# Optimization experiments

Measured on AMD Instinct MI355X. Metric: run time of the kernel, lower is better.

Reference implementation:

```python
import jax, jax.numpy as jnp
import numpy as np
from jax import lax

B_SZ, L, D, N = 4, 2048, 768, 16


def setup_inputs() -> dict:
    key = jax.random.key(0)
    ks = jax.random.split(key, 8)
    x = jax.random.normal(ks[0], (B_SZ, L, D), dtype=jnp.float32)
    # A_log init: log(repeat(arange(1, N+1), 'n -> d n'))
    A_log = jnp.log(jnp.tile(jnp.arange(1, N + 1, dtype=jnp.float32), (D, 1)))  # (D, N)
    sD = 1.0 / np.sqrt(D)
    Wb = jax.random.normal(ks[1], (N, D), dtype=jnp.float32) * sD
    bb = jax.random.normal(ks[2], (N,), dtype=jnp.float32) * sD
    Wc = jax.random.normal(ks[3], (N, D), dtype=jnp.float32) * sD
    bc = jax.random.normal(ks[4], (N,), dtype=jnp.float32) * sD
    W1 = jax.random.normal(ks[5], (1, D), dtype=jnp.float32) * sD
    b1 = jnp.zeros((1,), dtype=jnp.float32)
    Wd = jax.random.normal(ks[6], (D, 1), dtype=jnp.float32)
    bd = jax.random.normal(ks[7], (D,), dtype=jnp.float32)
    return {"x": x, "A_log": A_log, "Wb": Wb, "bb": bb, "Wc": Wc, "bc": bc,
            "W1": W1, "b1": b1, "Wd": Wd, "bd": bd}


def reference(x, A_log, Wb, bb, Wc, bc, W1, b1, Wd, bd):
    # x: (b, l, d)
    A = -jnp.exp(A_log)                                   # (d, n)
    Bp = x @ Wb.T + bb                                    # (b, l, n)
    C = x @ Wc.T + bc                                     # (b, l, n)
    s1 = x @ W1.T + b1                                    # (b, l, 1)
    delta = jax.nn.softplus(s1 @ Wd.T + bd)               # (b, l, d)
    deltaA = jnp.exp(jnp.einsum('bld,dn->bldn', delta, A))          # (b, l, d, n)
    deltaB_u = jnp.einsum('bld,bln,bld->bldn', delta, Bp, x)        # (b, l, d, n)

    def step(h, inputs):
        dA, dBu, c = inputs                               # (b,d,n),(b,d,n),(b,n)
        h = dA * h + dBu
        y = jnp.einsum('bdn,bn->bd', h, c)
        return h, y

    b, l, d = x.shape
    n = A_log.shape[1]
    h0 = jnp.zeros((b, d, n), dtype=x.dtype)
    _, ys = lax.scan(step, h0, (jnp.moveaxis(deltaA, 1, 0),
                                jnp.moveaxis(deltaB_u, 1, 0),
                                jnp.moveaxis(C, 1, 0)))
    return jnp.moveaxis(ys, 0, 1)                          # (b, l, d)
```

## Files before the change

### kernel.cpp

```cpp
#include <hip/hip_runtime.h>
#include <math.h>

#define B_SZ 4
#define LSEQ 2048
#define DDIM 768
#define NST  16
#define NROW (B_SZ * LSEQ)
#define NJ   33

#define NC   128
#define CS   (LSEQ / NC)

#define KSPL 32
#define KCH  (DDIM / KSPL)

__global__ __launch_bounds__(256) void proj_part_kernel(
    const float* __restrict__ x,
    const float* __restrict__ Wb, const float* __restrict__ Wc,
    const float* __restrict__ W1, float* __restrict__ part)
{
    const int row = blockIdx.x * 256 + threadIdx.x;
    const int s = blockIdx.y;
    const int k0 = s * KCH;

    float4 xv[6];
    const float* xp = x + (size_t)row * DDIM + k0;
    #pragma unroll
    for (int q = 0; q < 6; ++q) xv[q] = *(const float4*)(xp + q * 4);

    float acc[NJ];
    #pragma unroll
    for (int j = 0; j < NJ; ++j) {
        const float* wrow = (j < 16) ? (Wb + j * DDIM)
                          : (j < 32) ? (Wc + (j - 16) * DDIM)
                                     : W1;
        const float* wk = wrow + k0;
        float a = 0.f;
        #pragma unroll
        for (int q = 0; q < 6; ++q) {
            a = fmaf(xv[q].x, wk[q * 4 + 0], a);
            a = fmaf(xv[q].y, wk[q * 4 + 1], a);
            a = fmaf(xv[q].z, wk[q * 4 + 2], a);
            a = fmaf(xv[q].w, wk[q * 4 + 3], a);
        }
        acc[j] = a;
    }
    #pragma unroll
    for (int j = 0; j < NJ; ++j)
        part[((size_t)s * NJ + j) * NROW + row] = acc[j];
}

__global__ __launch_bounds__(256) void proj_reduce_kernel(
    const float* __restrict__ part,
    const float* __restrict__ bb, const float* __restrict__ bc,
    const float* __restrict__ b1,
    float* __restrict__ Bp, float* __restrict__ Cc, float* __restrict__ s1)
{
    const int idx = blockIdx.x * 256 + threadIdx.x;
    if (idx >= NJ * NROW) return;
    const int j = idx / NROW;
    const int row = idx % NROW;
    float a = 0.f;
    #pragma unroll 8
    for (int s = 0; s < KSPL; ++s)
        a += part[((size_t)s * NJ + j) * NROW + row];
    if (j < 16)      Bp[(size_t)row * NST + j] = a + bb[j];
    else if (j < 32) Cc[(size_t)row * NST + (j - 16)] = a + bc[j - 16];
    else             s1[row] = a + b1[0];
}

__device__ __forceinline__ float softplus_f(float z) {
    float t = __expf(-fabsf(z));
    return fmaxf(z, 0.f) + __logf(1.f + t);
}

__device__ __forceinline__ void powers16(float p, float* e) {
    e[0] = p;      e[1] = p * p;      e[2] = e[1] * p;   e[3] = e[1] * e[1];
    e[4] = e[3] * p;  e[5] = e[3] * e[1];  e[6] = e[3] * e[2];  e[7] = e[3] * e[3];
    e[8] = e[7] * p;  e[9] = e[7] * e[1];  e[10] = e[7] * e[2]; e[11] = e[7] * e[3];
    e[12] = e[7] * e[4]; e[13] = e[7] * e[5]; e[14] = e[7] * e[6]; e[15] = e[7] * e[7];
}

__device__ __forceinline__ bool a_structured(const float* acoef) {
    bool st = true;
    #pragma unroll
    for (int n = 0; n < NST; ++n)
        st = st && (fabsf(acoef[n] - (float)(n + 1) * acoef[0]) <= 1e-5f * fabsf(acoef[n]));
    return __all(st) != 0;
}

__global__ __launch_bounds__(256) void pass1_kernel(
    const float* __restrict__ x, const float* __restrict__ A_log,
    const float* __restrict__ Wd, const float* __restrict__ bd,
    const float* __restrict__ Bp, const float* __restrict__ s1,
    float* __restrict__ Ssum, float* __restrict__ Q)
{
    const int tid = threadIdx.x;
    const int d = blockIdx.x * 256 + tid;
    const int c = blockIdx.y, b = blockIdx.z;
    const int rowbase = b * LSEQ + c * CS;

    const float wd = Wd[d], bdv = bd[d];
    float acoef[NST];
    #pragma unroll
    for (int n = 0; n < NST; ++n) acoef[n] = -__expf(A_log[d * NST + n]);
    const float a0 = acoef[0];
    const bool structured = a_structured(acoef);

    const float4* B4 = (const float4*)(Bp + (size_t)rowbase * NST);
    const float* s1p = s1 + rowbase;
    const float* xp = x + (size_t)rowbase * DDIM + d;

    float h[NST];
    #pragma unroll
    for (int n = 0; n < NST; ++n) h[n] = 0.f;
    float S = 0.f;

    if (structured) {
        #pragma unroll 4
        for (int l = 0; l < CS; ++l) {
            const float delta = softplus_f(fmaf(s1p[l], wd, bdv));
            S += delta;
            float e[NST];
            powers16(__expf(delta * a0), e);
            const float dx = delta * xp[(size_t)l * DDIM];
            const float4 b0 = B4[l * 4 + 0], b1v = B4[l * 4 + 1];
            const float4 b2 = B4[l * 4 + 2], b3v = B4[l * 4 + 3];
            const float bv[NST] = {b0.x, b0.y, b0.z, b0.w, b1v.x, b1v.y, b1v.z, b1v.w,
                                   b2.x, b2.y, b2.z, b2.w, b3v.x, b3v.y, b3v.z, b3v.w};
            #pragma unroll
            for (int n = 0; n < NST; ++n) h[n] = fmaf(e[n], h[n], dx * bv[n]);
        }
    } else {
        #pragma unroll 4
        for (int l = 0; l < CS; ++l) {
            const float delta = softplus_f(fmaf(s1p[l], wd, bdv));
            S += delta;
            float e[NST];
            #pragma unroll
            for (int n = 0; n < NST; ++n) e[n] = __expf(delta * acoef[n]);
            const float dx = delta * xp[(size_t)l * DDIM];
            const float4 b0 = B4[l * 4 + 0], b1v = B4[l * 4 + 1];
            const float4 b2 = B4[l * 4 + 2], b3v = B4[l * 4 + 3];
            const float bv[NST] = {b0.x, b0.y, b0.z, b0.w, b1v.x, b1v.y, b1v.z, b1v.w,
                                   b2.x, b2.y, b2.z, b2.w, b3v.x, b3v.y, b3v.z, b3v.w};
            #pragma unroll
            for (int n = 0; n < NST; ++n) h[n] = fmaf(e[n], h[n], dx * bv[n]);
        }
    }
    Ssum[((size_t)b * NC + c) * DDIM + d] = S;
    const size_t gbase = (((size_t)b * NC + c) * DDIM + d) * NST;
    float4* Q4 = (float4*)(Q + gbase);
    #pragma unroll
    for (int q = 0; q < 4; ++q)
        Q4[q] = make_float4(h[q * 4], h[q * 4 + 1], h[q * 4 + 2], h[q * 4 + 3]);
}

#define CPG (NC / 4)
__global__ __launch_bounds__(256) void combine_kernel(
    const float* __restrict__ A_log,
    const float* __restrict__ Ssum, const float* __restrict__ Q,
    float* __restrict__ Hin)
{
    const int gidx = blockIdx.x * 256 + threadIdx.x;
    const int lane = threadIdx.x & 63;
    const int rlow = gidx & 15;
    const int g = (gidx >> 4) & 3;
    const int hi = gidx >> 6;
    const int pairIdx = hi * 16 + rlow;
    const int b = pairIdx / (DDIM * NST);
    const int r = pairIdx % (DDIM * NST);
    const int d = r >> 4;
    const float acoef = -__expf(A_log[r]);
    const int c0 = g * CPG;

    float eq[CPG], qq[CPG];
    #pragma unroll
    for (int ci = 0; ci < CPG; ++ci) {
        const size_t base = (size_t)(b * NC + c0 + ci);
        eq[ci] = __expf(acoef * Ssum[base * DDIM + d]);
        qq[ci] = Q[base * (DDIM * NST) + r];
    }
    float E = 1.f, H = 0.f;
    #pragma unroll
    for (int ci = 0; ci < CPG; ++ci) { H = fmaf(eq[ci], H, qq[ci]); E *= eq[ci]; }

    float oE = __shfl_up(E, 16, 64);
    float oH = __shfl_up(H, 16, 64);
    if (lane >= 16) { H = fmaf(E, oH, H); E *= oE; }
    oE = __shfl_up(E, 32, 64);
    oH = __shfl_up(H, 32, 64);
    if (lane >= 32) { H = fmaf(E, oH, H); E *= oE; }

    float hin = __shfl_up(H, 16, 64);
    if (g == 0) hin = 0.f;

    float h = hin;
    #pragma unroll
    for (int ci = 0; ci < CPG; ++ci) {
        const size_t base = (size_t)(b * NC + c0 + ci);
        Hin[base * (DDIM * NST) + r] = h;
        h = fmaf(eq[ci], h, qq[ci]);
    }
}

__global__ __launch_bounds__(256) void pass2_kernel(
    const float* __restrict__ x, const float* __restrict__ A_log,
    const float* __restrict__ Wd, const float* __restrict__ bd,
    const float* __restrict__ Bp, const float* __restrict__ Cc,
    const float* __restrict__ s1, const float* __restrict__ Hin,
    float* __restrict__ out)
{
    const int tid = threadIdx.x;
    const int d = blockIdx.x * 256 + tid;
    const int c = blockIdx.y, b = blockIdx.z;
    const int rowbase = b * LSEQ + c * CS;

    const float wd = Wd[d], bdv = bd[d];
    float acoef[NST];
    #pragma unroll
    for (int n = 0; n < NST; ++n) acoef[n] = -__expf(A_log[d * NST + n]);
    const float a0 = acoef[0];
    const bool structured = a_structured(acoef);

    const float4* B4 = (const float4*)(Bp + (size_t)rowbase * NST);
    const float4* C4 = (const float4*)(Cc + (size_t)rowbase * NST);
    const float* s1p = s1 + rowbase;
    const float* xp = x + (size_t)rowbase * DDIM + d;
    float* yp = out + (size_t)rowbase * DDIM + d;

    float h[NST];
    const size_t gbase = (((size_t)b * NC + c) * DDIM + d) * NST;
    const float4* H4 = (const float4*)(Hin + gbase);
    #pragma unroll
    for (int q = 0; q < 4; ++q) {
        const float4 hv = H4[q];
        h[q * 4] = hv.x; h[q * 4 + 1] = hv.y; h[q * 4 + 2] = hv.z; h[q * 4 + 3] = hv.w;
    }

    if (structured) {
        #pragma unroll 4
        for (int l = 0; l < CS; ++l) {
            const float delta = softplus_f(fmaf(s1p[l], wd, bdv));
            float e[NST];
            powers16(__expf(delta * a0), e);
            const float dx = delta * xp[(size_t)l * DDIM];
            const float4 b0 = B4[l * 4 + 0], b1v = B4[l * 4 + 1];
            const float4 b2 = B4[l * 4 + 2], b3v = B4[l * 4 + 3];
            const float4 c0 = C4[l * 4 + 0], c1v = C4[l * 4 + 1];
            const float4 c2 = C4[l * 4 + 2], c3v = C4[l * 4 + 3];
            const float bv[NST] = {b0.x, b0.y, b0.z, b0.w, b1v.x, b1v.y, b1v.z, b1v.w,
                                   b2.x, b2.y, b2.z, b2.w, b3v.x, b3v.y, b3v.z, b3v.w};
            const float cv[NST] = {c0.x, c0.y, c0.z, c0.w, c1v.x, c1v.y, c1v.z, c1v.w,
                                   c2.x, c2.y, c2.z, c2.w, c3v.x, c3v.y, c3v.z, c3v.w};
            float y = 0.f;
            #pragma unroll
            for (int n = 0; n < NST; ++n) {
                h[n] = fmaf(e[n], h[n], dx * bv[n]);
                y = fmaf(h[n], cv[n], y);
            }
            yp[(size_t)l * DDIM] = y;
        }
    } else {
        #pragma unroll 4
        for (int l = 0; l < CS; ++l) {
            const float delta = softplus_f(fmaf(s1p[l], wd, bdv));
            float e[NST];
            #pragma unroll
            for (int n = 0; n < NST; ++n) e[n] = __expf(delta * acoef[n]);
            const float dx = delta * xp[(size_t)l * DDIM];
            const float4 b0 = B4[l * 4 + 0], b1v = B4[l * 4 + 1];
            const float4 b2 = B4[l * 4 + 2], b3v = B4[l * 4 + 3];
            const float4 c0 = C4[l * 4 + 0], c1v = C4[l * 4 + 1];
            const float4 c2 = C4[l * 4 + 2], c3v = C4[l * 4 + 3];
            const float bv[NST] = {b0.x, b0.y, b0.z, b0.w, b1v.x, b1v.y, b1v.z, b1v.w,
                                   b2.x, b2.y, b2.z, b2.w, b3v.x, b3v.y, b3v.z, b3v.w};
            const float cv[NST] = {c0.x, c0.y, c0.z, c0.w, c1v.x, c1v.y, c1v.z, c1v.w,
                                   c2.x, c2.y, c2.z, c2.w, c3v.x, c3v.y, c3v.z, c3v.w};
            float y = 0.f;
            #pragma unroll
            for (int n = 0; n < NST; ++n) {
                h[n] = fmaf(e[n], h[n], dx * bv[n]);
                y = fmaf(h[n], cv[n], y);
            }
            yp[(size_t)l * DDIM] = y;
        }
    }
}

extern "C" void kernel_launch(void* const* d_in, const int* in_sizes, int n_in,
                              void* d_out, int out_size, void* d_ws, size_t ws_size,
                              hipStream_t stream) {
    const float* x     = (const float*)d_in[0];
    const float* A_log = (const float*)d_in[1];
    const float* Wb    = (const float*)d_in[2];
    const float* bb    = (const float*)d_in[3];
    const float* Wc    = (const float*)d_in[4];
    const float* bc    = (const float*)d_in[5];
    const float* W1    = (const float*)d_in[6];
    const float* b1    = (const float*)d_in[7];
    const float* Wd    = (const float*)d_in[8];
    const float* bd    = (const float*)d_in[9];
    float* out = (float*)d_out;

    float* ws = (float*)d_ws;
    const size_t partN = (size_t)KSPL * NJ * NROW;
    const size_t BpN = (size_t)NROW * NST;
    const size_t s1N = (size_t)NROW;
    const size_t sN  = (size_t)B_SZ * NC * DDIM;
    const size_t agg = (size_t)B_SZ * NC * DDIM * NST;

    float* part = ws;
    float* Bp   = part + partN;
    float* Cc   = Bp + BpN;
    float* s1   = Cc + BpN;
    float* Ssum = s1 + s1N;
    float* Q    = Ssum + sN;
    float* Hin  = Q + agg;

    dim3 gproj(NROW / 256, KSPL);
    proj_part_kernel<<<gproj, 256, 0, stream>>>(x, Wb, Wc, W1, part);
    proj_reduce_kernel<<<(NJ * NROW + 255) / 256, 256, 0, stream>>>(part, bb, bc, b1, Bp, Cc, s1);

    dim3 gscan(DDIM / 256, NC, B_SZ);
    pass1_kernel<<<gscan, 256, 0, stream>>>(x, A_log, Wd, bd, Bp, s1, Ssum, Q);

    combine_kernel<<<(B_SZ * DDIM * NST * 4) / 256, 256, 0, stream>>>(A_log, Ssum, Q, Hin);

    pass2_kernel<<<gscan, 256, 0, stream>>>(x, A_log, Wd, bd, Bp, Cc, s1, Hin, out);
}
```

Measured before the change: 155.1 us.

## Fuse chunked scan passes into one cooperative kernel with grid syncs

Merges pass1, combine and pass2 into a single cooperative kernel that uses grid-wide syncs between phases. This removes two kernel launch boundaries and computes A coefficients once per thread. To make the grid fit co-resident, the chunk count is halved to 64, which gives longer sequential chunks and fewer parallel blocks. The projection K-split is also halved. A fallback runs the old three-kernel path when cooperative launch is unavailable.

```diff
diff --git a/kernel.cpp b/kernel.cpp
--- a/kernel.cpp
+++ b/kernel.cpp
@@ -1,5 +1,8 @@
 #include <hip/hip_runtime.h>
+#include <hip/hip_cooperative_groups.h>
 #include <math.h>
+
+namespace cg = cooperative_groups;
 
 #define B_SZ 4
 #define LSEQ 2048
@@ -8,10 +11,11 @@
 #define NROW (B_SZ * LSEQ)
 #define NJ   33
 
-#define NC   128
+#define NC   64
 #define CS   (LSEQ / NC)
-
-#define KSPL 32
+#define CPG  (NC / 4)
+
+#define KSPL 16
 #define KCH  (DDIM / KSPL)
 
 __global__ __launch_bounds__(256) void proj_part_kernel(
@@ -23,10 +27,10 @@
     const int s = blockIdx.y;
     const int k0 = s * KCH;
 
-    float4 xv[6];
+    float4 xv[KCH / 4];
     const float* xp = x + (size_t)row * DDIM + k0;
     #pragma unroll
-    for (int q = 0; q < 6; ++q) xv[q] = *(const float4*)(xp + q * 4);
+    for (int q = 0; q < KCH / 4; ++q) xv[q] = *(const float4*)(xp + q * 4);
 
     float acc[NJ];
     #pragma unroll
@@ -37,7 +41,7 @@
         const float* wk = wrow + k0;
         float a = 0.f;
         #pragma unroll
-        for (int q = 0; q < 6; ++q) {
+        for (int q = 0; q < KCH / 4; ++q) {
             a = fmaf(xv[q].x, wk[q * 4 + 0], a);
             a = fmaf(xv[q].y, wk[q * 4 + 1], a);
             a = fmaf(xv[q].z, wk[q * 4 + 2], a);
@@ -61,7 +65,7 @@
     const int j = idx / NROW;
     const int row = idx % NROW;
     float a = 0.f;
-    #pragma unroll 8
+    #pragma unroll
     for (int s = 0; s < KSPL; ++s)
         a += part[((size_t)s * NJ + j) * NROW + row];
     if (j < 16)      Bp[(size_t)row * NST + j] = a + bb[j];
@@ -89,24 +93,15 @@
     return __all(st) != 0;
 }
 
-__global__ __launch_bounds__(256) void pass1_kernel(
-    const float* __restrict__ x, const float* __restrict__ A_log,
-    const float* __restrict__ Wd, const float* __restrict__ bd,
+__device__ __forceinline__ void phaseA_body(
+    int b, int c, int d,
+    const float* __restrict__ x, const float* __restrict__ Wd, const float* __restrict__ bd,
     const float* __restrict__ Bp, const float* __restrict__ s1,
+    const float* acoef, float a0, bool structured,
     float* __restrict__ Ssum, float* __restrict__ Q)
 {
-    const int tid = threadIdx.x;
-    const int d = blockIdx.x * 256 + tid;
-    const int c = blockIdx.y, b = blockIdx.z;
     const int rowbase = b * LSEQ + c * CS;
-
     const float wd = Wd[d], bdv = bd[d];
-    float acoef[NST];
-    #pragma unroll
-    for (int n = 0; n < NST; ++n) acoef[n] = -__expf(A_log[d * NST + n]);
-    const float a0 = acoef[0];
-    const bool structured = a_structured(acoef);
-
     const float4* B4 = (const float4*)(Bp + (size_t)rowbase * NST);
     const float* s1p = s1 + rowbase;
     const float* xp = x + (size_t)rowbase * DDIM + d;
@@ -156,29 +151,27 @@
         Q4[q] = make_float4(h[q * 4], h[q * 4 + 1], h[q * 4 + 2], h[q * 4 + 3]);
 }
 
-#define CPG (NC / 4)
-__global__ __launch_bounds__(256) void combine_kernel(
+__device__ __forceinline__ void phaseB_body(
+    int gidx, int lane,
     const float* __restrict__ A_log,
     const float* __restrict__ Ssum, const float* __restrict__ Q,
     float* __restrict__ Hin)
 {
-    const int gidx = blockIdx.x * 256 + threadIdx.x;
-    const int lane = threadIdx.x & 63;
     const int rlow = gidx & 15;
     const int g = (gidx >> 4) & 3;
     const int hi = gidx >> 6;
     const int pairIdx = hi * 16 + rlow;
-    const int b = pairIdx / (DDIM * NST);
+    const int b2 = pairIdx / (DDIM * NST);
     const int r = pairIdx % (DDIM * NST);
-    const int d = r >> 4;
-    const float acoef = -__expf(A_log[r]);
+    const int d2 = r >> 4;
+    const float ac = -__expf(A_log[r]);
     const int c0 = g * CPG;
 
     float eq[CPG], qq[CPG];
     #pragma unroll
     for (int ci = 0; ci < CPG; ++ci) {
-        const size_t base = (size_t)(b * NC + c0 + ci);
-        eq[ci] = __expf(acoef * Ssum[base * DDIM + d]);
+        const size_t base = (size_t)(b2 * NC + c0 + ci);
+        eq[ci] = __expf(ac * Ssum[base * DDIM + d2]);
         qq[ci] = Q[base * (DDIM * NST) + r];
     }
     float E = 1.f, H = 0.f;
@@ -198,31 +191,22 @@
     float h = hin;
     #pragma unroll
     for (int ci = 0; ci < CPG; ++ci) {
-        const size_t base = (size_t)(b * NC + c0 + ci);
+        const size_t base = (size_t)(b2 * NC + c0 + ci);
         Hin[base * (DDIM * NST) + r] = h;
         h = fmaf(eq[ci], h, qq[ci]);
     }
 }
 
-__global__ __launch_bounds__(256) void pass2_kernel(
-    const float* __restrict__ x, const float* __restrict__ A_log,
-    const float* __restrict__ Wd, const float* __restrict__ bd,
+__device__ __forceinline__ void phaseC_body(
+    int b, int c, int d,
+    const float* __restrict__ x, const float* __restrict__ Wd, const float* __restrict__ bd,
     const float* __restrict__ Bp, const float* __restrict__ Cc,
     const float* __restrict__ s1, const float* __restrict__ Hin,
+    const float* acoef, float a0, bool structured,
     float* __restrict__ out)
 {
-    const int tid = threadIdx.x;
-    const int d = blockIdx.x * 256 + tid;
-    const int c = blockIdx.y, b = blockIdx.z;
     const int rowbase = b * LSEQ + c * CS;
-
     const float wd = Wd[d], bdv = bd[d];
-    float acoef[NST];
-    #pragma unroll
-    for (int n = 0; n < NST; ++n) acoef[n] = -__expf(A_log[d * NST + n]);
-    const float a0 = acoef[0];
-    const bool structured = a_structured(acoef);
-
     const float4* B4 = (const float4*)(Bp + (size_t)rowbase * NST);
     const float4* C4 = (const float4*)(Cc + (size_t)rowbase * NST);
     const float* s1p = s1 + rowbase;
@@ -247,12 +231,12 @@
             const float dx = delta * xp[(size_t)l * DDIM];
             const float4 b0 = B4[l * 4 + 0], b1v = B4[l * 4 + 1];
             const float4 b2 = B4[l * 4 + 2], b3v = B4[l * 4 + 3];
-            const float4 c0 = C4[l * 4 + 0], c1v = C4[l * 4 + 1];
-            const float4 c2 = C4[l * 4 + 2], c3v = C4[l * 4 + 3];
+            const float4 c0v = C4[l * 4 + 0], c1v = C4[l * 4 + 1];
+            const float4 c2v = C4[l * 4 + 2], c3v = C4[l * 4 + 3];
             const float bv[NST] = {b0.x, b0.y, b0.z, b0.w, b1v.x, b1v.y, b1v.z, b1v.w,
                                    b2.x, b2.y, b2.z, b2.w, b3v.x, b3v.y, b3v.z, b3v.w};
-            const float cv[NST] = {c0.x, c0.y, c0.z, c0.w, c1v.x, c1v.y, c1v.z, c1v.w,
-                                   c2.x, c2.y, c2.z, c2.w, c3v.x, c3v.y, c3v.z, c3v.w};
+            const float cv[NST] = {c0v.x, c0v.y, c0v.z, c0v.w, c1v.x, c1v.y, c1v.z, c1v.w,
+                                   c2v.x, c2v.y, c2v.z, c2v.w, c3v.x, c3v.y, c3v.z, c3v.w};
             float y = 0.f;
             #pragma unroll
             for (int n = 0; n < NST; ++n) {
@@ -271,12 +255,12 @@
             const float dx = delta * xp[(size_t)l * DDIM];
             const float4 b0 = B4[l * 4 + 0], b1v = B4[l * 4 + 1];
             const float4 b2 = B4[l * 4 + 2], b3v = B4[l * 4 + 3];
-            const float4 c0 = C4[l * 4 + 0], c1v = C4[l * 4 + 1];
-            const float4 c2 = C4[l * 4 + 2], c3v = C4[l * 4 + 3];
+            const float4 c0v = C4[l * 4 + 0], c1v = C4[l * 4 + 1];
+            const float4 c2v = C4[l * 4 + 2], c3v = C4[l * 4 + 3];
             const float bv[NST] = {b0.x, b0.y, b0.z, b0.w, b1v.x, b1v.y, b1v.z, b1v.w,
                                    b2.x, b2.y, b2.z, b2.w, b3v.x, b3v.y, b3v.z, b3v.w};
-            const float cv[NST] = {c0.x, c0.y, c0.z, c0.w, c1v.x, c1v.y, c1v.z, c1v.w,
-                                   c2.x, c2.y, c2.z, c2.w, c3v.x, c3v.y, c3v.z, c3v.w};
+            const float cv[NST] = {c0v.x, c0v.y, c0v.z, c0v.w, c1v.x, c1v.y, c1v.z, c1v.w,
+                                   c2v.x, c2v.y, c2v.z, c2v.w, c3v.x, c3v.y, c3v.z, c3v.w};
             float y = 0.f;
             #pragma unroll
             for (int n = 0; n < NST; ++n) {
@@ -286,6 +270,85 @@
             yp[(size_t)l * DDIM] = y;
         }
     }
+}
+
+__global__ __launch_bounds__(256) void pass1_kernel(
+    const float* __restrict__ x, const float* __restrict__ A_log,
+    const float* __restrict__ Wd, const float* __restrict__ bd,
+    const float* __restrict__ Bp, const float* __restrict__ s1,
+    float* __restrict__ Ssum, float* __restrict__ Q)
+{
+    const int d = blockIdx.x * 256 + threadIdx.x;
+    const int c = blockIdx.y, b = blockIdx.z;
+    float acoef[NST];
+    #pragma unroll
+    for (int n = 0; n < NST; ++n) acoef[n] = -__expf(A_log[d * NST + n]);
+    const bool structured = a_structured(acoef);
+    phaseA_body(b, c, d, x, Wd, bd, Bp, s1, acoef, acoef[0], structured, Ssum, Q);
+}
+
+__global__ __launch_bounds__(256) void combine_kernel(
+    const float* __restrict__ A_log,
+    const float* __restrict__ Ssum, const float* __restrict__ Q,
+    float* __restrict__ Hin)
+{
+    const int gidx = blockIdx.x * 256 + threadIdx.x;
+    phaseB_body(gidx, threadIdx.x & 63, A_log, Ssum, Q, Hin);
+}
+
+__global__ __launch_bounds__(256) void pass2_kernel(
+    const float* __restrict__ x, const float* __restrict__ A_log,
+    const float* __restrict__ Wd, const float* __restrict__ bd,
+    const float* __restrict__ Bp, const float* __restrict__ Cc,
+    const float* __restrict__ s1, const float* __restrict__ Hin,
+    float* __restrict__ out)
+{
+    const int d = blockIdx.x * 256 + threadIdx.x;
+    const int c = blockIdx.y, b = blockIdx.z;
+    float acoef[NST];
+    #pragma unroll
+    for (int n = 0; n < NST; ++n) acoef[n] = -__expf(A_log[d * NST + n]);
+    const bool structured = a_structured(acoef);
+    phaseC_body(b, c, d, x, Wd, bd, Bp, Cc, s1, Hin, acoef, acoef[0], structured, out);
+}
+
+#define GRID_F (3 * B_SZ * NC)
+
+__global__ __launch_bounds__(256, 3) void fused_scan_kernel(
+    const float* __restrict__ x, const float* __restrict__ A_log,
+    const float* __restrict__ Wd, const float* __restrict__ bd,
+    const float* __restrict__ Bp, const float* __restrict__ Cc,
+    const float* __restrict__ s1,
+    float* __restrict__ Ssum, float* __restrict__ Q, float* __restrict__ Hin,
+    float* __restrict__ out)
+{
+    const int tid = threadIdx.x;
+    const int bx = blockIdx.x;
+    const int dblk = bx / (B_SZ * NC);
+    const int rem  = bx % (B_SZ * NC);
+    const int b    = rem / NC;
+    const int c    = rem % NC;
+    const int d    = dblk * 256 + tid;
+
+    float acoef[NST];
+    #pragma unroll
+    for (int n = 0; n < NST; ++n) acoef[n] = -__expf(A_log[d * NST + n]);
+    const float a0 = acoef[0];
+    const bool structured = a_structured(acoef);
+
+    phaseA_body(b, c, d, x, Wd, bd, Bp, s1, acoef, a0, structured, Ssum, Q);
+
+    __threadfence();
+    cg::this_grid().sync();
+    __threadfence();
+
+    phaseB_body(bx * 256 + tid, tid & 63, A_log, Ssum, Q, Hin);
+
+    __threadfence();
+    cg::this_grid().sync();
+    __threadfence();
+
+    phaseC_body(b, c, d, x, Wd, bd, Bp, Cc, s1, Hin, acoef, a0, structured, out);
 }
 
 extern "C" void kernel_launch(void* const* d_in, const int* in_sizes, int n_in,
@@ -322,10 +385,33 @@
     proj_part_kernel<<<gproj, 256, 0, stream>>>(x, Wb, Wc, W1, part);
     proj_reduce_kernel<<<(NJ * NROW + 255) / 256, 256, 0, stream>>>(part, bb, bc, b1, Bp, Cc, s1);
 
-    dim3 gscan(DDIM / 256, NC, B_SZ);
-    pass1_kernel<<<gscan, 256, 0, stream>>>(x, A_log, Wd, bd, Bp, s1, Ssum, Q);
-
-    combine_kernel<<<(B_SZ * DDIM * NST * 4) / 256, 256, 0, stream>>>(A_log, Ssum, Q, Hin);
-
-    pass2_kernel<<<gscan, 256, 0, stream>>>(x, A_log, Wd, bd, Bp, Cc, s1, Hin, out);
-}
+    static int coop_mode = -1;
+    if (coop_mode < 0) {
+        int dev = 0;
+        (void)hipGetDevice(&dev);
+        int coopAttr = 0;
+        (void)hipDeviceGetAttribute(&coopAttr, hipDeviceAttributeCooperativeLaunch, dev);
+        int ncu = 0;
+        (void)hipDeviceGetAttribute(&ncu, hipDeviceAttributeMultiprocessorCount, dev);
+        int nblk = 0;
+        hipError_t oe = hipOccupancyMaxActiveBlocksPerMultiprocessor(&nblk, fused_scan_kernel, 256, 0);
+        coop_mode = (coopAttr && oe == hipSuccess && (long)nblk * ncu >= GRID_F) ? 1 : 0;
+    }
+
+    bool done = false;
+    if (coop_mode == 1) {
+        void* kargs[] = {(void*)&x, (void*)&A_log, (void*)&Wd, (void*)&bd,
+                         (void*)&Bp, (void*)&Cc, (void*)&s1,
+                         (void*)&Ssum, (void*)&Q, (void*)&Hin, (void*)&out};
+        hipError_t le = hipLaunchCooperativeKernel((const void*)fused_scan_kernel,
+                                                   dim3(GRID_F), dim3(256), kargs, 0, stream);
+        if (le == hipSuccess) done = true;
+        else coop_mode = 0;
+    }
+    if (!done) {
+        dim3 gscan(DDIM / 256, NC, B_SZ);
+        pass1_kernel<<<gscan, 256, 0, stream>>>(x, A_log, Wd, bd, Bp, s1, Ssum, Q);
+        combine_kernel<<<(B_SZ * DDIM * NST * 4) / 256, 256, 0, stream>>>(A_log, Ssum, Q, Hin);
+        pass2_kernel<<<gscan, 256, 0, stream>>>(x, A_log, Wd, bd, Bp, Cc, s1, Hin, out);
+    }
+}
```

New measurement: 157.0 us. No clear change (+1.2%).

## Stage chunk inputs in shared memory and halve scan chunk and K-split counts

Applied to the files above, without the earlier changes.

The two scan passes now cooperatively load the chunk's x tile, B/C coefficients and s1 values into shared memory with vectorized float4 loads before the recurrence, instead of each thread issuing strided global loads per timestep. The chunk count drops from 128 to 64, giving longer chunks, a smaller Q/Hin aggregate buffer and a cheaper combine step. The projection K-split drops from 32 to 16, so each thread does more work per split and the partial-sum buffer and reduction shrink. In exchange there is less parallelism in the scan kernels, which may hurt latency hiding, and added LDS use (about 32KB per block) that limits occupancy.

```diff
diff --git a/kernel.cpp b/kernel.cpp
--- a/kernel.cpp
+++ b/kernel.cpp
@@ -8,10 +8,11 @@
 #define NROW (B_SZ * LSEQ)
 #define NJ   33
 
-#define NC   128
+#define NC   64
 #define CS   (LSEQ / NC)
-
-#define KSPL 32
+#define CPG  (NC / 4)
+
+#define KSPL 16
 #define KCH  (DDIM / KSPL)
 
 __global__ __launch_bounds__(256) void proj_part_kernel(
@@ -23,10 +24,10 @@
     const int s = blockIdx.y;
     const int k0 = s * KCH;
 
-    float4 xv[6];
+    float4 xv[KCH / 4];
     const float* xp = x + (size_t)row * DDIM + k0;
     #pragma unroll
-    for (int q = 0; q < 6; ++q) xv[q] = *(const float4*)(xp + q * 4);
+    for (int q = 0; q < KCH / 4; ++q) xv[q] = *(const float4*)(xp + q * 4);
 
     float acc[NJ];
     #pragma unroll
@@ -37,7 +38,7 @@
         const float* wk = wrow + k0;
         float a = 0.f;
         #pragma unroll
-        for (int q = 0; q < 6; ++q) {
+        for (int q = 0; q < KCH / 4; ++q) {
             a = fmaf(xv[q].x, wk[q * 4 + 0], a);
             a = fmaf(xv[q].y, wk[q * 4 + 1], a);
             a = fmaf(xv[q].z, wk[q * 4 + 2], a);
@@ -61,7 +62,7 @@
     const int j = idx / NROW;
     const int row = idx % NROW;
     float a = 0.f;
-    #pragma unroll 8
+    #pragma unroll
     for (int s = 0; s < KSPL; ++s)
         a += part[((size_t)s * NJ + j) * NROW + row];
     if (j < 16)      Bp[(size_t)row * NST + j] = a + bb[j];
@@ -95,10 +96,34 @@
     const float* __restrict__ Bp, const float* __restrict__ s1,
     float* __restrict__ Ssum, float* __restrict__ Q)
 {
+    __shared__ float xs[CS][256];
+    __shared__ float bs[CS][NST];
+    __shared__ float ss[CS];
+
     const int tid = threadIdx.x;
-    const int d = blockIdx.x * 256 + tid;
+    const int d0 = blockIdx.x * 256;
+    const int d = d0 + tid;
     const int c = blockIdx.y, b = blockIdx.z;
     const int rowbase = b * LSEQ + c * CS;
+
+    {
+        const float4* xg = (const float4*)(x + (size_t)rowbase * DDIM + d0);
+        #pragma unroll
+        for (int i = 0; i < (CS * 256 / 4) / 256; ++i) {
+            const int flat = i * 256 + tid;
+            const int r = flat >> 6, q = flat & 63;
+            const float4 v = xg[(size_t)r * (DDIM / 4) + q];
+            float* p = &xs[r][q * 4];
+            p[0] = v.x; p[1] = v.y; p[2] = v.z; p[3] = v.w;
+        }
+        if (tid < CS * NST / 4) {
+            const float4 v = ((const float4*)(Bp + (size_t)rowbase * NST))[tid];
+            const int r = tid >> 2, q = tid & 3;
+            float* p = &bs[r][q * 4];
+            p[0] = v.x; p[1] = v.y; p[2] = v.z; p[3] = v.w;
+        }
+        if (tid < CS) ss[tid] = s1[rowbase + tid];
+    }
 
     const float wd = Wd[d], bdv = bd[d];
     float acoef[NST];
@@ -107,9 +132,7 @@
     const float a0 = acoef[0];
     const bool structured = a_structured(acoef);
 
-    const float4* B4 = (const float4*)(Bp + (size_t)rowbase * NST);
-    const float* s1p = s1 + rowbase;
-    const float* xp = x + (size_t)rowbase * DDIM + d;
+    __syncthreads();
 
     float h[NST];
     #pragma unroll
@@ -119,13 +142,15 @@
     if (structured) {
         #pragma unroll 4
         for (int l = 0; l < CS; ++l) {
-            const float delta = softplus_f(fmaf(s1p[l], wd, bdv));
+            const float delta = softplus_f(fmaf(ss[l], wd, bdv));
             S += delta;
             float e[NST];
             powers16(__expf(delta * a0), e);
-            const float dx = delta * xp[(size_t)l * DDIM];
-            const float4 b0 = B4[l * 4 + 0], b1v = B4[l * 4 + 1];
-            const float4 b2 = B4[l * 4 + 2], b3v = B4[l * 4 + 3];
+            const float dx = delta * xs[l][tid];
+            const float4 b0 = *(const float4*)&bs[l][0];
+            const float4 b1v = *(const float4*)&bs[l][4];
+            const float4 b2 = *(const float4*)&bs[l][8];
+            const float4 b3v = *(const float4*)&bs[l][12];
             const float bv[NST] = {b0.x, b0.y, b0.z, b0.w, b1v.x, b1v.y, b1v.z, b1v.w,
                                    b2.x, b2.y, b2.z, b2.w, b3v.x, b3v.y, b3v.z, b3v.w};
             #pragma unroll
@@ -134,14 +159,16 @@
     } else {
         #pragma unroll 4
         for (int l = 0; l < CS; ++l) {
-            const float delta = softplus_f(fmaf(s1p[l], wd, bdv));
+            const float delta = softplus_f(fmaf(ss[l], wd, bdv));
             S += delta;
             float e[NST];
             #pragma unroll
             for (int n = 0; n < NST; ++n) e[n] = __expf(delta * acoef[n]);
-            const float dx = delta * xp[(size_t)l * DDIM];
-            const float4 b0 = B4[l * 4 + 0], b1v = B4[l * 4 + 1];
-            const float4 b2 = B4[l * 4 + 2], b3v = B4[l * 4 + 3];
+            const float dx = delta * xs[l][tid];
+            const float4 b0 = *(const float4*)&bs[l][0];
+            const float4 b1v = *(const float4*)&bs[l][4];
+            const float4 b2 = *(const float4*)&bs[l][8];
+            const float4 b3v = *(const float4*)&bs[l][12];
             const float bv[NST] = {b0.x, b0.y, b0.z, b0.w, b1v.x, b1v.y, b1v.z, b1v.w,
                                    b2.x, b2.y, b2.z, b2.w, b3v.x, b3v.y, b3v.z, b3v.w};
             #pragma unroll
@@ -156,7 +183,6 @@
         Q4[q] = make_float4(h[q * 4], h[q * 4 + 1], h[q * 4 + 2], h[q * 4 + 3]);
 }
 
-#define CPG (NC / 4)
 __global__ __launch_bounds__(256) void combine_kernel(
     const float* __restrict__ A_log,
     const float* __restrict__ Ssum, const float* __restrict__ Q,
@@ -168,17 +194,17 @@
     const int g = (gidx >> 4) & 3;
     const int hi = gidx >> 6;
     const int pairIdx = hi * 16 + rlow;
-    const int b = pairIdx / (DDIM * NST);
+    const int b2 = pairIdx / (DDIM * NST);
     const int r = pairIdx % (DDIM * NST);
-    const int d = r >> 4;
-    const float acoef = -__expf(A_log[r]);
+    const int d2 = r >> 4;
+    const float ac = -__expf(A_log[r]);
     const int c0 = g * CPG;
 
     float eq[CPG], qq[CPG];
     #pragma unroll
     for (int ci = 0; ci < CPG; ++ci) {
-        const size_t base = (size_t)(b * NC + c0 + ci);
-        eq[ci] = __expf(acoef * Ssum[base * DDIM + d]);
+        const size_t base = (size_t)(b2 * NC + c0 + ci);
+        eq[ci] = __expf(ac * Ssum[base * DDIM + d2]);
         qq[ci] = Q[base * (DDIM * NST) + r];
     }
     float E = 1.f, H = 0.f;
@@ -198,7 +224,7 @@
     float h = hin;
     #pragma unroll
     for (int ci = 0; ci < CPG; ++ci) {
-        const size_t base = (size_t)(b * NC + c0 + ci);
+        const size_t base = (size_t)(b2 * NC + c0 + ci);
         Hin[base * (DDIM * NST) + r] = h;
         h = fmaf(eq[ci], h, qq[ci]);
     }
@@ -211,10 +237,41 @@
     const float* __restrict__ s1, const float* __restrict__ Hin,
     float* __restrict__ out)
 {
+    __shared__ float xs[CS][256];
+    __shared__ float bs[CS][NST];
+    __shared__ float cs[CS][NST];
+    __shared__ float ss[CS];
+
     const int tid = threadIdx.x;
-    const int d = blockIdx.x * 256 + tid;
+    const int d0 = blockIdx.x * 256;
+    const int d = d0 + tid;
     const int c = blockIdx.y, b = blockIdx.z;
     const int rowbase = b * LSEQ + c * CS;
+
+    {
+        const float4* xg = (const float4*)(x + (size_t)rowbase * DDIM + d0);
+        #pragma unroll
+        for (int i = 0; i < (CS * 256 / 4) / 256; ++i) {
+            const int flat = i * 256 + tid;
+            const int r = flat >> 6, q = flat & 63;
+            const float4 v = xg[(size_t)r * (DDIM / 4) + q];
+            float* p = &xs[r][q * 4];
+            p[0] = v.x; p[1] = v.y; p[2] = v.z; p[3] = v.w;
+        }
+        if (tid < CS * NST / 4) {
+            const float4 v = ((const float4*)(Bp + (size_t)rowbase * NST))[tid];
+            const int r = tid >> 2, q = tid & 3;
+            float* p = &bs[r][q * 4];
+            p[0] = v.x; p[1] = v.y; p[2] = v.z; p[3] = v.w;
+        } else {
+            const int t2 = tid - 128;
+            const float4 v = ((const float4*)(Cc + (size_t)rowbase * NST))[t2];
+            const int r = t2 >> 2, q = t2 & 3;
+            float* p = &cs[r][q * 4];
+            p[0] = v.x; p[1] = v.y; p[2] = v.z; p[3] = v.w;
+        }
+        if (tid < CS) ss[tid] = s1[rowbase + tid];
+    }
 
     const float wd = Wd[d], bdv = bd[d];
     float acoef[NST];
@@ -223,12 +280,6 @@
     const float a0 = acoef[0];
     const bool structured = a_structured(acoef);
 
-    const float4* B4 = (const float4*)(Bp + (size_t)rowbase * NST);
-    const float4* C4 = (const float4*)(Cc + (size_t)rowbase * NST);
-    const float* s1p = s1 + rowbase;
-    const float* xp = x + (size_t)rowbase * DDIM + d;
-    float* yp = out + (size_t)rowbase * DDIM + d;
-
     float h[NST];
     const size_t gbase = (((size_t)b * NC + c) * DDIM + d) * NST;
     const float4* H4 = (const float4*)(Hin + gbase);
@@ -238,21 +289,29 @@
         h[q * 4] = hv.x; h[q * 4 + 1] = hv.y; h[q * 4 + 2] = hv.z; h[q * 4 + 3] = hv.w;
     }
 
+    __syncthreads();
+
+    float* yp = out + (size_t)rowbase * DDIM + d;
+
     if (structured) {
         #pragma unroll 4
         for (int l = 0; l < CS; ++l) {
-            const float delta = softplus_f(fmaf(s1p[l], wd, bdv));
+            const float delta = softplus_f(fmaf(ss[l], wd, bdv));
             float e[NST];
             powers16(__expf(delta * a0), e);
-            const float dx = delta * xp[(size_t)l * DDIM];
-            const float4 b0 = B4[l * 4 + 0], b1v = B4[l * 4 + 1];
-            const float4 b2 = B4[l * 4 + 2], b3v = B4[l * 4 + 3];
-            const float4 c0 = C4[l * 4 + 0], c1v = C4[l * 4 + 1];
-            const float4 c2 = C4[l * 4 + 2], c3v = C4[l * 4 + 3];
+            const float dx = delta * xs[l][tid];
+            const float4 b0 = *(const float4*)&bs[l][0];
+            const float4 b1v = *(const float4*)&bs[l][4];
+            const float4 b2 = *(const float4*)&bs[l][8];
+            const float4 b3v = *(const float4*)&bs[l][12];
+            const float4 c0v = *(const float4*)&cs[l][0];
+            const float4 c1v = *(const float4*)&cs[l][4];
+            const float4 c2v = *(const float4*)&cs[l][8];
+            const float4 c3v = *(const float4*)&cs[l][12];
             const float bv[NST] = {b0.x, b0.y, b0.z, b0.w, b1v.x, b1v.y, b1v.z, b1v.w,
                                    b2.x, b2.y, b2.z, b2.w, b3v.x, b3v.y, b3v.z, b3v.w};
-            const float cv[NST] = {c0.x, c0.y, c0.z, c0.w, c1v.x, c1v.y, c1v.z, c1v.w,
-                                   c2.x, c2.y, c2.z, c2.w, c3v.x, c3v.y, c3v.z, c3v.w};
+            const float cv[NST] = {c0v.x, c0v.y, c0v.z, c0v.w, c1v.x, c1v.y, c1v.z, c1v.w,
+                                   c2v.x, c2v.y, c2v.z, c2v.w, c3v.x, c3v.y, c3v.z, c3v.w};
             float y = 0.f;
             #pragma unroll
             for (int n = 0; n < NST; ++n) {
@@ -264,19 +323,23 @@
     } else {
         #pragma unroll 4
         for (int l = 0; l < CS; ++l) {
-            const float delta = softplus_f(fmaf(s1p[l], wd, bdv));
+            const float delta = softplus_f(fmaf(ss[l], wd, bdv));
             float e[NST];
             #pragma unroll
             for (int n = 0; n < NST; ++n) e[n] = __expf(delta * acoef[n]);
-            const float dx = delta * xp[(size_t)l * DDIM];
-            const float4 b0 = B4[l * 4 + 0], b1v = B4[l * 4 + 1];
-            const float4 b2 = B4[l * 4 + 2], b3v = B4[l * 4 + 3];
-            const float4 c0 = C4[l * 4 + 0], c1v = C4[l * 4 + 1];
-            const float4 c2 = C4[l * 4 + 2], c3v = C4[l * 4 + 3];
+            const float dx = delta * xs[l][tid];
+            const float4 b0 = *(const float4*)&bs[l][0];
+            const float4 b1v = *(const float4*)&bs[l][4];
+            const float4 b2 = *(const float4*)&bs[l][8];
+            const float4 b3v = *(const float4*)&bs[l][12];
+            const float4 c0v = *(const float4*)&cs[l][0];
+            const float4 c1v = *(const float4*)&cs[l][4];
+            const float4 c2v = *(const float4*)&cs[l][8];
+            const float4 c3v = *(const float4*)&cs[l][12];
             const float bv[NST] = {b0.x, b0.y, b0.z, b0.w, b1v.x, b1v.y, b1v.z, b1v.w,
                                    b2.x, b2.y, b2.z, b2.w, b3v.x, b3v.y, b3v.z, b3v.w};
-            const float cv[NST] = {c0.x, c0.y, c0.z, c0.w, c1v.x, c1v.y, c1v.z, c1v.w,
-                                   c2.x, c2.y, c2.z, c2.w, c3v.x, c3v.y, c3v.z, c3v.w};
+            const float cv[NST] = {c0v.x, c0v.y, c0v.z, c0v.w, c1v.x, c1v.y, c1v.z, c1v.w,
+                                   c2v.x, c2v.y, c2v.z, c2v.w, c3v.x, c3v.y, c3v.z, c3v.w};
             float y = 0.f;
             #pragma unroll
             for (int n = 0; n < NST; ++n) {
@@ -324,8 +387,6 @@
 
     dim3 gscan(DDIM / 256, NC, B_SZ);
     pass1_kernel<<<gscan, 256, 0, stream>>>(x, A_log, Wd, bd, Bp, s1, Ssum, Q);
-
     combine_kernel<<<(B_SZ * DDIM * NST * 4) / 256, 256, 0, stream>>>(A_log, Ssum, Q, Hin);
-
     pass2_kernel<<<gscan, 256, 0, stream>>>(x, A_log, Wd, bd, Bp, Cc, s1, Hin, out);
 }
```

Measured after the change: 160.0 us. 1.03x slower.
